# Kernel optimization log

Measured on AMD Instinct MI355X. Metric: run time of the kernel, lower is better.

## Reference

```python
import jax, jax.numpy as jnp
import numpy as np

B, T, C, H = 4, 4096, 1024, 128

def setup_inputs() -> dict:
    key = jax.random.key(0)
    kx, kk, kq, kv = jax.random.split(key, 4)
    x = jax.random.normal(kx, (B, T, C), dtype=jnp.float32)
    # torch nn.Linear(C, H, bias=False) stored here as [C, H] so y = x @ W
    s = 1.0 / np.sqrt(C)
    w_key = jax.random.uniform(kk, (C, H), jnp.float32, -s, s)
    w_query = jax.random.uniform(kq, (C, H), jnp.float32, -s, s)
    w_value = jax.random.uniform(kv, (C, H), jnp.float32, -s, s)
    return {"x": x, "w_key": w_key, "w_query": w_query, "w_value": w_value}

def reference(x, w_key, w_query, w_value):
    # Single-head causal self-attention (dropout p=0.0 -> identity).
    k = x @ w_key      # [B,T,H]
    q = x @ w_query    # [B,T,H]
    v = x @ w_value    # [B,T,H]
    scale = k.shape[-1] ** -0.5
    scores = jnp.einsum('bqh,bkh->bqk', q, k) * scale  # [B,T,T]
    causal = jnp.tril(jnp.ones((x.shape[1], x.shape[1]), dtype=bool))
    scores = jnp.where(causal, scores, -jnp.inf)
    attn = jax.nn.softmax(scores, axis=-1)
    return jnp.einsum('bqk,bkh->bqh', attn, v)  # [B,T,H]
```

## Files before the change

kernel.cpp:

```cpp
#include <hip/hip_runtime.h>
#include <hip/hip_bf16.h>


typedef unsigned short u16;
typedef __attribute__((ext_vector_type(8))) __bf16 bf16x8;
typedef __attribute__((ext_vector_type(8))) u16 u16x8;
typedef __attribute__((ext_vector_type(4))) u16 u16x4;
typedef __attribute__((ext_vector_type(4))) float f32x4;

#define T_DIM 4096
#define C_DIM 1024
#define H_DIM 128
#define EPB 272
#define WS_SPLIT_NEED 50135040ull

static __device__ __forceinline__ f32x4 mfma16x16(u16x8 a, u16x8 b, f32x4 c) {
  return __builtin_amdgcn_mfma_f32_16x16x32_bf16(
      __builtin_bit_cast(bf16x8, a), __builtin_bit_cast(bf16x8, b), c, 0, 0, 0);
}

static __device__ __forceinline__ u16 f2bf(float f) {
  __hip_bfloat16 h = __float2bfloat16(f);
  return __builtin_bit_cast(u16, h);
}

static __device__ __forceinline__ float bf2f(u16 u) {
  unsigned x = (unsigned)u << 16;
  return __builtin_bit_cast(float, x);
}

static __device__ __forceinline__ void gll16(const u16* g, u16* l) {
  __builtin_amdgcn_global_load_lds(
      (const __attribute__((address_space(1))) void*)(void*)g,
      (__attribute__((address_space(3))) void*)l, 16, 0, 0);
}

__global__ __launch_bounds__(256) void prep_w_kernel(
    const float* __restrict__ wk, const float* __restrict__ wq,
    const float* __restrict__ wv, u16* __restrict__ Wt) {
  __shared__ u16 L[64 * 136];
  const int w = blockIdx.y;
  const int k0 = blockIdx.x * 64;
  const float* W = (w == 0) ? wk : (w == 1) ? wq : wv;
  const int t = threadIdx.x;
#pragma unroll
  for (int p = 0; p < 8; ++p) {
    int idx = p * 256 + t;
    int k = idx >> 5, c4 = (idx & 31) * 4;
    float4 v = *(const float4*)&W[(size_t)(k0 + k) * H_DIM + c4];
    u16x4 bv;
    bv.x = f2bf(v.x); bv.y = f2bf(v.y); bv.z = f2bf(v.z); bv.w = f2bf(v.w);
    *(u16x4*)&L[k * 136 + c4] = bv;
  }
  __syncthreads();
#pragma unroll
  for (int p = 0; p < 4; ++p) {
    int cid = p * 256 + t;
    int n = cid >> 3, kc = (cid & 7) * 8;
    u16x8 o;
#pragma unroll
    for (int j = 0; j < 8; ++j) o[j] = L[(kc + j) * 136 + n];
    *(u16x8*)&Wt[(size_t)w * 131072 + (size_t)n * 1024 + k0 + kc] = o;
  }
}

__global__ __launch_bounds__(256, 2) void proj_kernel(
    const float* __restrict__ x, const u16* __restrict__ Wt,
    u16* __restrict__ Qb, u16* __restrict__ Kb, u16* __restrict__ Vt) {
  __shared__ __attribute__((aligned(16))) u16 smem[32 * 72 + 384 * 64];
  u16* Xl = smem;
  u16* Wl = smem + 32 * 72;
  const int m0 = blockIdx.x * 32;
  const int t = threadIdx.x;
  const int wave = t >> 6, lane = t & 63;
  const int g = lane >> 4, lq = lane & 15;
  const int lsw = lq & 7;

  f32x4 acc[2][6] = {};

  for (int k0 = 0; k0 < C_DIM; k0 += 64) {
    __syncthreads();
#pragma unroll
    for (int p = 0; p < 2; ++p) {
      int idx = p * 256 + t;
      int row = idx >> 4, c4 = (idx & 15) * 4;
      float4 v = *(const float4*)&x[(size_t)(m0 + row) * C_DIM + k0 + c4];
      u16x4 bv;
      bv.x = f2bf(v.x); bv.y = f2bf(v.y); bv.z = f2bf(v.z); bv.w = f2bf(v.w);
      *(u16x4*)&Xl[row * 72 + c4] = bv;
    }
#pragma unroll
    for (int p = 0; p < 12; ++p) {
      int r0 = (wave * 12 + p) * 8;
      int r = r0 + (lane >> 3);
      int csrc = (lane & 7) ^ (lane >> 3);
      gll16(&Wt[(size_t)(r >> 7) * 131072 + (size_t)(r & 127) * 1024 + k0 +
                csrc * 8],
            &Wl[r0 * 64]);
    }
    __syncthreads();
#pragma unroll
    for (int kk = 0; kk < 2; ++kk) {
      u16x8 af[2], bfr[6];
#pragma unroll
      for (int i = 0; i < 2; ++i)
        af[i] = *(const u16x8*)&Xl[(i * 16 + lq) * 72 + kk * 32 + g * 8];
#pragma unroll
      for (int j = 0; j < 6; ++j)
        bfr[j] = *(const u16x8*)&Wl[(wave * 96 + j * 16 + lq) * 64 +
                                    (((kk * 4 + g) ^ lsw) * 8)];
#pragma unroll
      for (int i = 0; i < 2; ++i)
#pragma unroll
        for (int j = 0; j < 6; ++j)
          acc[i][j] = mfma16x16(af[i], bfr[j], acc[i][j]);
    }
  }

  const float qscale = 0.08838834764831845f;
#pragma unroll
  for (int j = 0; j < 6; ++j) {
    const int c384 = wave * 96 + j * 16;
    const int which = c384 >> 7;
    const int col = (c384 & 127) + lq;
    if (which == 0) {
#pragma unroll
      for (int i = 0; i < 2; ++i)
#pragma unroll
        for (int r = 0; r < 4; ++r)
          Kb[(size_t)(m0 + i * 16 + g * 4 + r) * H_DIM + col] =
              f2bf(acc[i][j][r]);
    } else if (which == 1) {
#pragma unroll
      for (int i = 0; i < 2; ++i)
#pragma unroll
        for (int r = 0; r < 4; ++r)
          Qb[(size_t)(m0 + i * 16 + g * 4 + r) * H_DIM + col] =
              f2bf(acc[i][j][r] * qscale);
    }
  }
  __syncthreads();
#pragma unroll
  for (int j = 0; j < 6; ++j) {
    const int c384 = wave * 96 + j * 16;
    if ((c384 >> 7) == 2) {
      const int v = (c384 & 127) + lq;
#pragma unroll
      for (int i = 0; i < 2; ++i)
#pragma unroll
        for (int r = 0; r < 4; ++r)
          smem[v * 40 + i * 16 + g * 4 + r] = f2bf(acc[i][j][r]);
    }
  }
  __syncthreads();
  {
    const int b = m0 >> 12;
    const int t0 = m0 & 4095;
#pragma unroll
    for (int p = 0; p < 2; ++p) {
      int idx = p * 256 + t;
      int h = idx >> 2, mc = (idx & 3) * 8;
      *(u16x8*)&Vt[(size_t)b * (H_DIM * T_DIM) + (size_t)h * T_DIM + t0 + mc] =
          *(const u16x8*)&smem[h * 40 + mc];
    }
  }
}

__global__ __launch_bounds__(512, 4) void attn_kernel(
    const u16* __restrict__ Qb, const u16* __restrict__ Kb,
    const u16* __restrict__ Vt, float* __restrict__ out,
    u16* __restrict__ Opart, float* __restrict__ ml, int split) {
  __shared__ __attribute__((aligned(16))) u16 Kl[64 * 128];
  __shared__ __attribute__((aligned(16))) u16 Vl[128 * 64];
  __shared__ __attribute__((aligned(16))) u16 Pl[8][16 * 72];
  const int t = threadIdx.x;
  const int wave = t >> 6, lane = t & 63;
  const int g = lane >> 4, lq = lane & 15;
  const int lsw = lane & 7;

  int b, qb, kvb, kve, pid;
  if (split) {
    int bid = (int)blockIdx.x;
    int xcd = bid & 7;
    b = xcd >> 1;
    int e = (EPB - 1) - ((bid >> 3) * 2 + (bid & 1));
    int a = 0;
#pragma unroll
    for (int c = 1; c <= 15; ++c)
      if (e >= c * (c + 1)) a = c;
    int off = e - a * (a + 1);
    int d = off / (a + 1);
    int ch = off - d * (a + 1);
    qb = 2 * a + d;
    kvb = ch * 256;
    pid = b * EPB + e;
    int kv_full = qb * 128 + 128;
    kve = (kvb + 256 < kv_full) ? kvb + 256 : kv_full;
  } else {
    b = (int)blockIdx.x & 3;
    qb = 31 - ((int)blockIdx.x >> 2);
    kvb = 0;
    kve = qb * 128 + 128;
    pid = 0;
  }
  const int rowq = qb * 128 + wave * 16;
  const int qrow = rowq + lq;

  u16x8 qf[4];
  {
    const u16* Qp = Qb + (size_t)(b * T_DIM + qrow) * H_DIM;
#pragma unroll
    for (int c = 0; c < 4; ++c) qf[c] = *(const u16x8*)&Qp[c * 32 + g * 8];
  }

  f32x4 ao[8] = {};
  float m_run = -INFINITY, l_run = 0.f;

  const u16* Kg0 = Kb + (size_t)b * T_DIM * H_DIM;
  const u16* Vg0 = Vt + (size_t)b * H_DIM * T_DIM;

  for (int kv0 = kvb; kv0 < kve; kv0 += 64) {
    __syncthreads();
#pragma unroll
    for (int i = 0; i < 2; ++i) {
      int r0 = (i * 8 + wave) * 4;
      int r = r0 + (lane >> 4);
      int csrc = (lane & 15) ^ (r & 7);
      gll16(&Kg0[(size_t)(kv0 + r) * H_DIM + csrc * 8], &Kl[r0 * 128]);
    }
#pragma unroll
    for (int i = 0; i < 2; ++i) {
      int h0 = (i * 8 + wave) * 8;
      int h = h0 + (lane >> 3);
      int csrc = (lane & 7) ^ (lane >> 3);
      gll16(&Vg0[(size_t)h * T_DIM + kv0 + csrc * 8], &Vl[h0 * 64]);
    }
    __syncthreads();

    if (kv0 > rowq + 15) continue;

    f32x4 s[4];
#pragma unroll
    for (int nf = 0; nf < 4; ++nf) s[nf] = f32x4{0.f, 0.f, 0.f, 0.f};
#pragma unroll
    for (int nf = 0; nf < 4; ++nf)
#pragma unroll
      for (int c = 0; c < 4; ++c) {
        u16x8 kf = *(const u16x8*)&Kl[(nf * 16 + lq) * 128 +
                                      (((c * 4 + g) ^ lsw) * 8)];
        s[nf] = mfma16x16(kf, qf[c], s[nf]);
      }

    if (kv0 + 63 > rowq) {
      const int kb = kv0 + g * 4;
#pragma unroll
      for (int nf = 0; nf < 4; ++nf)
#pragma unroll
        for (int r = 0; r < 4; ++r)
          if (kb + nf * 16 + r > qrow) s[nf][r] = -INFINITY;
    }

    float t0 = fmaxf(fmaxf(s[0][0], s[0][1]), fmaxf(s[0][2], s[0][3]));
    float t1 = fmaxf(fmaxf(s[1][0], s[1][1]), fmaxf(s[1][2], s[1][3]));
    float t2 = fmaxf(fmaxf(s[2][0], s[2][1]), fmaxf(s[2][2], s[2][3]));
    float t3 = fmaxf(fmaxf(s[3][0], s[3][1]), fmaxf(s[3][2], s[3][3]));
    float pmax = fmaxf(fmaxf(t0, t1), fmaxf(t2, t3));
    pmax = fmaxf(pmax, __shfl_xor(pmax, 16));
    pmax = fmaxf(pmax, __shfl_xor(pmax, 32));

    float mn = fmaxf(m_run, pmax);
    float al = __expf(m_run - mn);
    m_run = mn;
#pragma unroll
    for (int nf = 0; nf < 4; ++nf)
#pragma unroll
      for (int r = 0; r < 4; ++r) s[nf][r] = __expf(s[nf][r] - mn);
    float u0 = (s[0][0] + s[0][1]) + (s[0][2] + s[0][3]);
    float u1 = (s[1][0] + s[1][1]) + (s[1][2] + s[1][3]);
    float u2 = (s[2][0] + s[2][1]) + (s[2][2] + s[2][3]);
    float u3 = (s[3][0] + s[3][1]) + (s[3][2] + s[3][3]);
    float ps = (u0 + u1) + (u2 + u3);
    ps += __shfl_xor(ps, 16);
    ps += __shfl_xor(ps, 32);
    l_run = l_run * al + ps;

    if (!__all(al == 1.f)) {
      float alr[4];
#pragma unroll
      for (int r = 0; r < 4; ++r) alr[r] = __shfl(al, g * 4 + r);
#pragma unroll
      for (int h8 = 0; h8 < 8; ++h8)
#pragma unroll
        for (int r = 0; r < 4; ++r) ao[h8][r] *= alr[r];
    }

#pragma unroll
    for (int nf = 0; nf < 4; ++nf)
#pragma unroll
      for (int r = 0; r < 4; ++r)
        Pl[wave][lq * 72 + nf * 16 + g * 4 + r] = f2bf(s[nf][r]);

    u16x8 pf[2];
#pragma unroll
    for (int kk = 0; kk < 2; ++kk)
      pf[kk] = *(const u16x8*)&Pl[wave][lq * 72 + kk * 32 + g * 8];
#pragma unroll
    for (int h8 = 0; h8 < 8; ++h8)
#pragma unroll
      for (int kk = 0; kk < 2; ++kk) {
        u16x8 vf = *(const u16x8*)&Vl[(h8 * 16 + lq) * 64 +
                                      (((kk * 4 + g) ^ lsw) * 8)];
        ao[h8] = mfma16x16(pf[kk], vf, ao[h8]);
      }
  }

  if (!split) {
    float linv = 1.f / l_run;
    float inv[4];
#pragma unroll
    for (int r = 0; r < 4; ++r) inv[r] = __shfl(linv, g * 4 + r);
    float* Og = out + (size_t)(b * T_DIM + rowq) * H_DIM;
#pragma unroll
    for (int h8 = 0; h8 < 8; ++h8)
#pragma unroll
      for (int r = 0; r < 4; ++r)
        Og[(size_t)(g * 4 + r) * H_DIM + h8 * 16 + lq] = ao[h8][r] * inv[r];
  } else {
    u16* Op = Opart + (size_t)pid * 16384 + (size_t)(wave * 16) * H_DIM;
#pragma unroll
    for (int h8 = 0; h8 < 8; ++h8)
#pragma unroll
      for (int r = 0; r < 4; ++r)
        Op[(g * 4 + r) * H_DIM + h8 * 16 + lq] = f2bf(ao[h8][r]);
    if (lane < 16) {
      float* mlp = ml + (size_t)pid * 256;
      mlp[wave * 16 + lane] = m_run;
      mlp[128 + wave * 16 + lane] = l_run;
    }
  }
}

__global__ __launch_bounds__(256) void combine_kernel(
    const u16* __restrict__ Opart, const float* __restrict__ ml,
    float* __restrict__ out) {
  const int blk = blockIdx.x;
  const int qb = blk >> 2;
  const int sub = blk & 3;
  const int b = blockIdx.y;
  const int t = threadIdx.x;
  const int row = sub * 32 + (t >> 3);
  const int colb = (t & 7) * 16;
  const int a = qb >> 1;
  const int n = a + 1;
  const int base = a * (a + 1) + (qb & 1) * (a + 1);
  const int pid0 = b * EPB + base;

  float M = -INFINITY;
  for (int i = 0; i < n; ++i)
    M = fmaxf(M, ml[(size_t)(pid0 + i) * 256 + row]);

  float L = 0.f;
  float o[16] = {};
  for (int i = 0; i < n; ++i) {
    const size_t mb = (size_t)(pid0 + i) * 256;
    float sc = __expf(ml[mb + row] - M);
    L += sc * ml[mb + 128 + row];
    const u16* Op = Opart + (size_t)(pid0 + i) * 16384 + row * H_DIM + colb;
#pragma unroll
    for (int p = 0; p < 2; ++p) {
      u16x8 v = *(const u16x8*)&Op[p * 8];
#pragma unroll
      for (int e = 0; e < 8; ++e) o[p * 8 + e] += sc * bf2f(v[e]);
    }
  }
  float inv = 1.f / L;
  float* Og = out + ((size_t)b * T_DIM + qb * 128 + row) * H_DIM + colb;
#pragma unroll
  for (int p = 0; p < 4; ++p) {
    f32x4 v = {o[p * 4] * inv, o[p * 4 + 1] * inv, o[p * 4 + 2] * inv,
               o[p * 4 + 3] * inv};
    *(f32x4*)&Og[p * 4] = v;
  }
}

extern "C" void kernel_launch(void* const* d_in, const int* in_sizes, int n_in,
                              void* d_out, int out_size, void* d_ws,
                              size_t ws_size, hipStream_t stream) {
  const float* x = (const float*)d_in[0];
  const float* wk = (const float*)d_in[1];
  const float* wq = (const float*)d_in[2];
  const float* wv = (const float*)d_in[3];
  float* out = (float*)d_out;
  char* ws = (char*)d_ws;

  u16* Wt = (u16*)ws;
  u16* Qb = (u16*)(ws + 786432);
  u16* Kb = (u16*)(ws + 786432 + 4194304);
  u16* Vt = (u16*)(ws + 786432 + 8388608);
  u16* Opart = (u16*)(ws + 13369344);
  float* ml = (float*)(ws + 49020928);

  const int split = (ws_size >= WS_SPLIT_NEED) ? 1 : 0;

  prep_w_kernel<<<dim3(16, 3), 256, 0, stream>>>(wk, wq, wv, Wt);
  proj_kernel<<<512, 256, 0, stream>>>(x, Wt, Qb, Kb, Vt);
  if (split) {
    attn_kernel<<<4 * EPB, 512, 0, stream>>>(Qb, Kb, Vt, out, Opart, ml, 1);
    combine_kernel<<<dim3(128, 4), 256, 0, stream>>>(Opart, ml, out);
  } else {
    attn_kernel<<<128, 512, 0, stream>>>(Qb, Kb, Vt, out, Opart, ml, 0);
  }
}
```

Baseline: 87.31 us.

## Pre-swizzle weights into MFMA fragment layout and stage full X tile once

The weight prep kernel now writes bf16 weights directly in per-lane MFMA B-fragment order, with the query scale folded into the weights. The projection kernel reads B fragments straight from global memory with no LDS staging. It converts the block's whole 32x1024 X tile to bf16 into LDS once, with an XOR swizzle, so the per-k-step syncs and staging loads go away. The cost is a 64KB LDS footprint, which may cut occupancy below two blocks per CU, and B-operand reads now depend on L2/L1 bandwidth.

```diff
diff --git a/kernel.cpp b/kernel.cpp
--- a/kernel.cpp
+++ b/kernel.cpp
@@ -37,78 +37,65 @@
 
 __global__ __launch_bounds__(256) void prep_w_kernel(
     const float* __restrict__ wk, const float* __restrict__ wq,
-    const float* __restrict__ wv, u16* __restrict__ Wt) {
-  __shared__ u16 L[64 * 136];
-  const int w = blockIdx.y;
-  const int k0 = blockIdx.x * 64;
+    const float* __restrict__ wv, u16* __restrict__ Wf) {
+  const int oid = blockIdx.x * 256 + threadIdx.x;
+  const int w = oid >> 14;
+  const int r = oid & 16383;
+  const int nb = r >> 11;
+  const int kb = (r >> 6) & 31;
+  const int lane = r & 63;
+  const int g = lane >> 4, lq = lane & 15;
   const float* W = (w == 0) ? wk : (w == 1) ? wq : wv;
-  const int t = threadIdx.x;
-#pragma unroll
-  for (int p = 0; p < 8; ++p) {
-    int idx = p * 256 + t;
-    int k = idx >> 5, c4 = (idx & 31) * 4;
-    float4 v = *(const float4*)&W[(size_t)(k0 + k) * H_DIM + c4];
-    u16x4 bv;
-    bv.x = f2bf(v.x); bv.y = f2bf(v.y); bv.z = f2bf(v.z); bv.w = f2bf(v.w);
-    *(u16x4*)&L[k * 136 + c4] = bv;
-  }
-  __syncthreads();
-#pragma unroll
-  for (int p = 0; p < 4; ++p) {
-    int cid = p * 256 + t;
-    int n = cid >> 3, kc = (cid & 7) * 8;
-    u16x8 o;
-#pragma unroll
-    for (int j = 0; j < 8; ++j) o[j] = L[(kc + j) * 136 + n];
-    *(u16x8*)&Wt[(size_t)w * 131072 + (size_t)n * 1024 + k0 + kc] = o;
-  }
+  const float sc = (w == 1) ? 0.08838834764831845f : 1.0f;
+  const int k0 = kb * 32 + g * 8;
+  const int n = nb * 16 + lq;
+  u16x8 o;
+#pragma unroll
+  for (int j = 0; j < 8; ++j) o[j] = f2bf(W[(size_t)(k0 + j) * H_DIM + n] * sc);
+  *(u16x8*)&Wf[(size_t)oid * 8] = o;
 }
 
 __global__ __launch_bounds__(256, 2) void proj_kernel(
-    const float* __restrict__ x, const u16* __restrict__ Wt,
+    const float* __restrict__ x, const u16* __restrict__ Wf,
     u16* __restrict__ Qb, u16* __restrict__ Kb, u16* __restrict__ Vt) {
-  __shared__ __attribute__((aligned(16))) u16 smem[32 * 72 + 384 * 64];
-  u16* Xl = smem;
-  u16* Wl = smem + 32 * 72;
+  __shared__ __attribute__((aligned(16))) u16 smem[32 * 1024];
   const int m0 = blockIdx.x * 32;
   const int t = threadIdx.x;
   const int wave = t >> 6, lane = t & 63;
   const int g = lane >> 4, lq = lane & 15;
   const int lsw = lq & 7;
 
+#pragma unroll
+  for (int p = 0; p < 16; ++p) {
+    int c = p * 256 + t;
+    int row = c >> 7, cc = c & 127;
+    const float* xp = &x[(size_t)(m0 + row) * C_DIM + cc * 8];
+    float4 v0 = *(const float4*)xp;
+    float4 v1 = *(const float4*)(xp + 4);
+    u16x8 bv;
+    bv[0] = f2bf(v0.x); bv[1] = f2bf(v0.y); bv[2] = f2bf(v0.z); bv[3] = f2bf(v0.w);
+    bv[4] = f2bf(v1.x); bv[5] = f2bf(v1.y); bv[6] = f2bf(v1.z); bv[7] = f2bf(v1.w);
+    *(u16x8*)&smem[row * 1024 + ((cc ^ (row & 7)) * 8)] = bv;
+  }
+  __syncthreads();
+
   f32x4 acc[2][6] = {};
 
   for (int k0 = 0; k0 < C_DIM; k0 += 64) {
-    __syncthreads();
-#pragma unroll
-    for (int p = 0; p < 2; ++p) {
-      int idx = p * 256 + t;
-      int row = idx >> 4, c4 = (idx & 15) * 4;
-      float4 v = *(const float4*)&x[(size_t)(m0 + row) * C_DIM + k0 + c4];
-      u16x4 bv;
-      bv.x = f2bf(v.x); bv.y = f2bf(v.y); bv.z = f2bf(v.z); bv.w = f2bf(v.w);
-      *(u16x4*)&Xl[row * 72 + c4] = bv;
-    }
-#pragma unroll
-    for (int p = 0; p < 12; ++p) {
-      int r0 = (wave * 12 + p) * 8;
-      int r = r0 + (lane >> 3);
-      int csrc = (lane & 7) ^ (lane >> 3);
-      gll16(&Wt[(size_t)(r >> 7) * 131072 + (size_t)(r & 127) * 1024 + k0 +
-                csrc * 8],
-            &Wl[r0 * 64]);
-    }
-    __syncthreads();
+    const int kb0 = k0 >> 5;
 #pragma unroll
     for (int kk = 0; kk < 2; ++kk) {
       u16x8 af[2], bfr[6];
 #pragma unroll
       for (int i = 0; i < 2; ++i)
-        af[i] = *(const u16x8*)&Xl[(i * 16 + lq) * 72 + kk * 32 + g * 8];
-#pragma unroll
-      for (int j = 0; j < 6; ++j)
-        bfr[j] = *(const u16x8*)&Wl[(wave * 96 + j * 16 + lq) * 64 +
-                                    (((kk * 4 + g) ^ lsw) * 8)];
+        af[i] = *(const u16x8*)&smem[(i * 16 + lq) * 1024 +
+                                     ((((k0 >> 3) + kk * 4 + g) ^ lsw) * 8)];
+#pragma unroll
+      for (int j = 0; j < 6; ++j) {
+        int nb = wave * 6 + j;
+        bfr[j] = *(const u16x8*)&Wf[(size_t)(nb * 32 + kb0 + kk) * 512 +
+                                    lane * 8];
+      }
 #pragma unroll
       for (int i = 0; i < 2; ++i)
 #pragma unroll
@@ -117,7 +104,6 @@
     }
   }
 
-  const float qscale = 0.08838834764831845f;
 #pragma unroll
   for (int j = 0; j < 6; ++j) {
     const int c384 = wave * 96 + j * 16;
@@ -136,7 +122,7 @@
 #pragma unroll
         for (int r = 0; r < 4; ++r)
           Qb[(size_t)(m0 + i * 16 + g * 4 + r) * H_DIM + col] =
-              f2bf(acc[i][j][r] * qscale);
+              f2bf(acc[i][j][r]);
     }
   }
   __syncthreads();
@@ -393,7 +379,7 @@
   float* out = (float*)d_out;
   char* ws = (char*)d_ws;
 
-  u16* Wt = (u16*)ws;
+  u16* Wf = (u16*)ws;
   u16* Qb = (u16*)(ws + 786432);
   u16* Kb = (u16*)(ws + 786432 + 4194304);
   u16* Vt = (u16*)(ws + 786432 + 8388608);
@@ -402,8 +388,8 @@
 
   const int split = (ws_size >= WS_SPLIT_NEED) ? 1 : 0;
 
-  prep_w_kernel<<<dim3(16, 3), 256, 0, stream>>>(wk, wq, wv, Wt);
-  proj_kernel<<<512, 256, 0, stream>>>(x, Wt, Qb, Kb, Vt);
+  prep_w_kernel<<<192, 256, 0, stream>>>(wk, wq, wv, Wf);
+  proj_kernel<<<512, 256, 0, stream>>>(x, Wf, Qb, Kb, Vt);
   if (split) {
     attn_kernel<<<4 * EPB, 512, 0, stream>>>(Qb, Kb, Vt, out, Opart, ml, 1);
     combine_kernel<<<dim3(128, 4), 256, 0, stream>>>(Opart, ml, out);
```

After: 96.25 us. +10.2%, slower.
